# Kernel optimization log

Measured on AMD Instinct MI355X. Metric: run time of the kernel, lower is better.

The kernel has to match this reference:

```python
import jax, jax.numpy as jnp
import numpy as np

N, H, F, E, K = 4096, 512, 2048, 8, 2  # tokens, hidden, ffn(=4H), experts, top_k


def setup_inputs() -> dict:
    key = jax.random.key(0)
    ks = jax.random.split(key, 7)
    def w(k, shape, fan_in):
        return jax.random.normal(k, shape, dtype=jnp.float32) * (fan_in ** -0.5)
    return {
        "x": jax.random.normal(ks[0], (N, H), dtype=jnp.float32),
        "W_in": w(ks[1], (H, H), H),          # input_proj.weight  [out,in]
        "W_router": w(ks[2], (E, H), H),      # router.gate.weight [E,H]
        "W_gate": w(ks[3], (E, F, H), H),     # per-expert gate_proj.weight
        "W_up": w(ks[4], (E, F, H), H),       # per-expert up_proj.weight
        "W_down": w(ks[5], (E, H, F), F),     # per-expert down_proj.weight
        "W_out": w(ks[6], (H, H), H),         # output_proj.weight
    }


def reference(x, W_in, W_router, W_gate, W_up, W_down, W_out):
    h = x @ W_in.T                                  # [N,H] input_proj
    logits = h @ W_router.T                         # [N,E]
    # route_mode='balanced' and world_size==1 -> expert_bias is None
    probs = jax.nn.softmax(logits, axis=-1)
    top_w, top_i = jax.lax.top_k(probs, K)          # [N,K]
    top_w = jax.nn.softmax(top_w, axis=-1)          # renormalize over top-k

    # per-token combine weight for each expert: [N,E]
    onehot = jax.nn.one_hot(top_i, E, dtype=h.dtype)      # [N,K,E]
    combine_w = jnp.einsum('nk,nke->ne', top_w, onehot)

    def expert(wg, wu, wd):
        # SwiGLU FFN: down( silu(gate(h)) * up(h) )
        return (jax.nn.silu(h @ wg.T) * (h @ wu.T)) @ wd.T  # [N,H]

    expert_out = jax.vmap(expert)(W_gate, W_up, W_down)     # [E,N,H]
    combined = jnp.einsum('ne,enh->nh', combine_w, expert_out)
    return combined @ W_out.T                                # output_proj
```

## Files before the change

### kernel.cpp

```cpp
#include <hip/hip_runtime.h>

typedef unsigned short u16;
typedef unsigned int u32;
typedef short bf16x8 __attribute__((ext_vector_type(8)));
typedef float f32x4 __attribute__((ext_vector_type(4)));

#define AS1 __attribute__((address_space(1)))
#define AS3 __attribute__((address_space(3)))

#define NTOK 4096
#define HDIM 512
#define FDIM 2048
#define NEXP 8
#define NASSIGN (NTOK * 2)
#define NPAD2 (NASSIGN + NEXP * 256)
#define RBMAX 128

__device__ __forceinline__ void g2l16(const void* g, void* l) {
  __builtin_amdgcn_global_load_lds((const AS1 u32*)g, (AS3 u32*)l, 16, 0, 0);
}
__device__ __forceinline__ u16 f2bf(float f) {
  u32 u = __float_as_uint(f);
  u = (u + 0x7FFFu + ((u >> 16) & 1u)) >> 16;
  return (u16)u;
}
__device__ __forceinline__ float bf2f(u16 h) { return __uint_as_float(((u32)h) << 16); }

#define WAITV0() asm volatile("s_waitcnt vmcnt(0)" ::: "memory")
#define BAR() __builtin_amdgcn_s_barrier()
#define SCB() __builtin_amdgcn_sched_barrier(0)
#define PRIO1() __builtin_amdgcn_s_setprio(1)
#define PRIO0() __builtin_amdgcn_s_setprio(0)
#define VMBAR() do { WAITV0(); BAR(); } while (0)

__global__ __launch_bounds__(256) void cvtall_kernel(
    const float* __restrict__ x, const float* __restrict__ Wi, const float* __restrict__ Wo,
    const float* __restrict__ Wg, const float* __restrict__ Wu, const float* __restrict__ Wd,
    const float* __restrict__ Wr,
    u16* __restrict__ xb, u16* __restrict__ Wib, u16* __restrict__ Wob,
    u16* __restrict__ Wgb, u16* __restrict__ Wub, u16* __restrict__ Wdb,
    double* __restrict__ wre) {
  const int b = blockIdx.x, tid = threadIdx.x;
  if (b < 6784) {
    const int b4 = b * 1024;
    const float* s; u16* d; int o;
    if (b4 < 524288) { s = x; d = xb; o = b4; }
    else if (b4 < 589824) { s = Wi; d = Wib; o = b4 - 524288; }
    else if (b4 < 655360) { s = Wo; d = Wob; o = b4 - 589824; }
    else if (b4 < 2752512) { s = Wg; d = Wgb; o = b4 - 655360; }
    else if (b4 < 4849664) { s = Wu; d = Wub; o = b4 - 2752512; }
    else { s = Wd; d = Wdb; o = b4 - 4849664; }
    const int oo = o + tid;
    const float4 v0 = ((const float4*)s)[oo];
    const float4 v1 = ((const float4*)s)[oo + 256];
    const float4 v2 = ((const float4*)s)[oo + 512];
    const float4 v3 = ((const float4*)s)[oo + 768];
    ushort4 t0, t1, t2, t3;
    t0.x = f2bf(v0.x); t0.y = f2bf(v0.y); t0.z = f2bf(v0.z); t0.w = f2bf(v0.w);
    t1.x = f2bf(v1.x); t1.y = f2bf(v1.y); t1.z = f2bf(v1.z); t1.w = f2bf(v1.w);
    t2.x = f2bf(v2.x); t2.y = f2bf(v2.y); t2.z = f2bf(v2.z); t2.w = f2bf(v2.w);
    t3.x = f2bf(v3.x); t3.y = f2bf(v3.y); t3.z = f2bf(v3.z); t3.w = f2bf(v3.w);
    ((ushort4*)d)[oo] = t0;
    ((ushort4*)d)[oo + 256] = t1;
    ((ushort4*)d)[oo + 512] = t2;
    ((ushort4*)d)[oo + 768] = t3;
  } else {
    const int t = (b - 6784) * 256 + tid;
    const int e = t >> 9, k = t & 511;
    const float* wr = Wr + e * HDIM;
    double a0 = 0.0, a1 = 0.0, a2 = 0.0, a3 = 0.0;
    for (int j = 0; j < HDIM; j += 4) {
      a0 += (double)wr[j + 0] * (double)Wi[(j + 0) * HDIM + k];
      a1 += (double)wr[j + 1] * (double)Wi[(j + 1) * HDIM + k];
      a2 += (double)wr[j + 2] * (double)Wi[(j + 2) * HDIM + k];
      a3 += (double)wr[j + 3] * (double)Wi[(j + 3) * HDIM + k];
    }
    wre[t] = (a0 + a1) + (a2 + a3);
  }
}

__global__ __launch_bounds__(128) void router_kernel(
    const float* __restrict__ x, const double* __restrict__ wre,
    int* __restrict__ idx, float* __restrict__ wts) {
  __shared__ double lw[NEXP * HDIM];
  for (int i = threadIdx.x; i < NEXP * HDIM; i += 128) lw[i] = wre[i];
  __syncthreads();
  const int n = blockIdx.x * 128 + threadIdx.x;
  const float* xr = x + (size_t)n * HDIM;
  double acc[NEXP] = {};
  for (int k4 = 0; k4 < HDIM / 4; ++k4) {
    const float4 xv = ((const float4*)xr)[k4];
    const float xc[4] = {xv.x, xv.y, xv.z, xv.w};
#pragma unroll
    for (int c = 0; c < 4; ++c) {
      const double xd = (double)xc[c];
#pragma unroll
      for (int e = 0; e < NEXP; ++e) acc[e] += xd * lw[e * HDIM + k4 * 4 + c];
    }
  }
  double mx = acc[0];
#pragma unroll
  for (int e = 1; e < NEXP; ++e) mx = acc[e] > mx ? acc[e] : mx;
  double p[NEXP], se = 0.0;
#pragma unroll
  for (int e = 0; e < NEXP; ++e) { p[e] = exp(acc[e] - mx); se += p[e]; }
  const double inv = 1.0 / se;
#pragma unroll
  for (int e = 0; e < NEXP; ++e) p[e] *= inv;
  int i0 = 0; double b0 = p[0];
#pragma unroll
  for (int e = 1; e < NEXP; ++e) if (p[e] > b0) { b0 = p[e]; i0 = e; }
  int i1 = -1; double b1 = -1.0;
#pragma unroll
  for (int e = 0; e < NEXP; ++e) if (e != i0 && p[e] > b1) { b1 = p[e]; i1 = e; }
  const double e0 = exp(b0), e1 = exp(b1);
  idx[2 * n] = i0; idx[2 * n + 1] = i1;
  wts[2 * n] = (float)(e0 / (e0 + e1));
  wts[2 * n + 1] = (float)(e1 / (e0 + e1));
}

__global__ void assign_kernel(const int* __restrict__ idx, int* __restrict__ tok,
                              int* __restrict__ pos, int* __restrict__ rbe2,
                              int* __restrict__ rbp2, int* __restrict__ rbe1,
                              int* __restrict__ rbp1, int* __restrict__ nrb) {
  __shared__ int cnt[NEXP], cur[NEXP];
  const int tid = threadIdx.x;
  if (tid < NEXP) cnt[tid] = 0;
  __syncthreads();
  for (int a = tid; a < NASSIGN; a += 256) atomicAdd(&cnt[idx[a]], 1);
  __syncthreads();
  if (tid == 0) {
    int o = 0, n2 = 0, n1 = 0;
    for (int e = 0; e < NEXP; ++e) {
      cur[e] = o;
      const int nb2 = (cnt[e] + 255) >> 8;
      const int nb1 = (cnt[e] + 127) >> 7;
      for (int i = 0; i < nb2; ++i) { rbe2[n2] = e; rbp2[n2] = o + i * 256; ++n2; }
      for (int i = 0; i < nb1; ++i) { rbe1[n1] = e; rbp1[n1] = o + i * 128; ++n1; }
      o += nb2 * 256;
    }
    nrb[0] = n2; nrb[1] = n1;
  }
  __syncthreads();
  for (int p = tid; p < NPAD2; p += 256) tok[p] = 0;
  __syncthreads();
  for (int a = tid; a < NASSIGN; a += 256) {
    const int e = idx[a];
    const int q = atomicAdd(&cur[e], 1);
    tok[q] = a >> 1;
    pos[a] = q;
  }
}

template <int SB, int NT>
__device__ __forceinline__ void gemm128_body(
    const u16* __restrict__ A, const u16* __restrict__ B, void* __restrict__ C,
    int m0, int n0, int N, int K, u16* sm, int tid) {
  u16 *lA0 = sm, *lA1 = sm + 8192, *lB0 = sm + 16384, *lB1 = sm + 24576;
  const int w = tid >> 6, l = tid & 63;
  const int wm = (w >> 2) * 64, wn = (w & 3) * 32;
  const int lm = l & 15, lk = (l >> 4) * 8, xr = (l & 7) << 3;
  const int sr = l >> 3, sc = ((l & 7) ^ sr) * 8;
  const u16* As = A + (size_t)(m0 + w * 8 + sr) * K + sc;
  const u16* Bs = B + (size_t)(n0 + w * 8 + sr) * K + sc;
  f32x4 acc[4][2] = {};
  auto STG = [&](u16* dA, u16* dB, int kt) {
    g2l16(As + kt, dA + w * 512);
    g2l16(As + (size_t)64 * K + kt, dA + 4096 + w * 512);
    g2l16(Bs + kt, dB + w * 512);
    g2l16(Bs + (size_t)64 * K + kt, dB + 4096 + w * 512);
  };
  auto CMP = [&](const u16* a_, const u16* b_) {
#pragma unroll
    for (int kk = 0; kk < 2; ++kk) {
      const int ko = (kk * 32 + lk) ^ xr;
      bf16x8 af[4], bf[2];
#pragma unroll
      for (int i = 0; i < 4; ++i) af[i] = *(const bf16x8*)(a_ + (wm + i * 16 + lm) * 64 + ko);
#pragma unroll
      for (int j = 0; j < 2; ++j) bf[j] = *(const bf16x8*)(b_ + (wn + j * 16 + lm) * 64 + ko);
#pragma unroll
      for (int i = 0; i < 4; ++i)
#pragma unroll
        for (int j = 0; j < 2; ++j)
          acc[i][j] = __builtin_amdgcn_mfma_f32_16x16x32_bf16(af[i], bf[j], acc[i][j], 0, 0, 0);
    }
  };
  STG(lA0, lB0, 0);
  VMBAR();
  for (int t = 0; t < NT; t += 2) {
    if (t + 1 < NT) STG(lA1, lB1, (t + 1) * 64);
    CMP(lA0, lB0);
    VMBAR();
    if (t + 2 < NT) STG(lA0, lB0, (t + 2) * 64);
    CMP(lA1, lB1);
    VMBAR();
  }
  const int cr = (l >> 4) * 4, cc = lm;
#pragma unroll
  for (int i = 0; i < 4; ++i)
#pragma unroll
    for (int j = 0; j < 2; ++j)
#pragma unroll
      for (int r = 0; r < 4; ++r) {
        const size_t o = (size_t)(m0 + wm + i * 16 + cr + r) * N + n0 + wn + j * 16 + cc;
        if (SB) ((u16*)C)[o] = f2bf(acc[i][j][r]);
        else ((float*)C)[o] = acc[i][j][r];
      }
}

__global__ __launch_bounds__(512, 2) void ingemm_kernel(
    const u16* __restrict__ xb, const u16* __restrict__ Wib, u16* __restrict__ hb) {
  __shared__ __align__(16) u16 sm[32768];
  gemm128_body<1, 8>(xb, Wib, hb, blockIdx.y * 128, blockIdx.x * 128, HDIM, HDIM, sm, threadIdx.x);
}

__global__ __launch_bounds__(512, 2) void outgemm_kernel(
    const u16* __restrict__ cb, const u16* __restrict__ Wob, float* __restrict__ out) {
  __shared__ __align__(16) u16 sm[32768];
  gemm128_body<0, 8>(cb, Wob, out, blockIdx.y * 128, blockIdx.x * 128, HDIM, HDIM, sm, threadIdx.x);
}

__global__ __launch_bounds__(512, 2) void gateup_kernel(
    const u16* __restrict__ hb, const u16* __restrict__ Wg, const u16* __restrict__ Wu,
    u16* __restrict__ act, const int* __restrict__ tok, const int* __restrict__ rbe2,
    const int* __restrict__ rbp2, const int* __restrict__ nrb) {
  const int rb = blockIdx.y;
  if (rb >= nrb[0]) return;
  __shared__ __align__(16) u16 sm[65536];
  const int e = rbe2[rb], p0 = rbp2[rb], n0 = blockIdx.x * 128;
  const int tid = threadIdx.x, w = tid >> 6, l = tid & 63;
  const int wr = w >> 1, wc = w & 1;
  const int lm = l & 15, lk = (l >> 4) * 8, xr = (l & 7) * 8;
  const int sr = l >> 3, sc = ((l & 7) ^ sr) * 8;
  const int ko0 = lk ^ xr, ko1 = (32 + lk) ^ xr;
  const u16* Asrc[4];
#pragma unroll
  for (int c = 0; c < 4; ++c)
    Asrc[c] = hb + (size_t)tok[p0 + c * 64 + w * 8 + sr] * HDIM + sc;
  const u16 *Gsrc[2], *Usrc[2];
#pragma unroll
  for (int c = 0; c < 2; ++c) {
    Gsrc[c] = Wg + (size_t)e * FDIM * HDIM + (size_t)(n0 + c * 64 + w * 8 + sr) * HDIM + sc;
    Usrc[c] = Wu + (size_t)e * FDIM * HDIM + (size_t)(n0 + c * 64 + w * 8 + sr) * HDIM + sc;
  }
  f32x4 ag[4][4] = {}, au[4][4] = {};
  auto stgA = [&](int b, int kt) {
#pragma unroll
    for (int c = 0; c < 4; ++c) g2l16(Asrc[c] + kt, sm + b * 32768 + c * 4096 + w * 512);
  };
  auto stgGU = [&](int b, int kt) {
#pragma unroll
    for (int c = 0; c < 2; ++c) {
      g2l16(Gsrc[c] + kt, sm + b * 32768 + 16384 + c * 4096 + w * 512);
      g2l16(Usrc[c] + kt, sm + b * 32768 + 24576 + c * 4096 + w * 512);
    }
  };
  stgA(0, 0); stgGU(0, 0);
  WAITV0(); BAR(); SCB();
#pragma unroll 2
  for (int t = 0; t < 8; ++t) {
    const int bu = t & 1, bn = bu ^ 1;
    const u16* A_ = sm + bu * 32768;
    const u16* G_ = A_ + 16384;
    const u16* U_ = A_ + 24576;
    bf16x8 af[4], gf[4], uf[4];
#pragma unroll
    for (int i = 0; i < 4; ++i) af[i] = *(const bf16x8*)(A_ + (wr * 64 + i * 16 + lm) * 64 + ko0);
#pragma unroll
    for (int j = 0; j < 4; ++j) gf[j] = *(const bf16x8*)(G_ + (wc * 64 + j * 16 + lm) * 64 + ko0);
    if (t < 7) stgA(bn, (t + 1) * 64);
    PRIO1();
#pragma unroll
    for (int i = 0; i < 4; ++i)
#pragma unroll
      for (int j = 0; j < 4; ++j)
        ag[i][j] = __builtin_amdgcn_mfma_f32_16x16x32_bf16(af[i], gf[j], ag[i][j], 0, 0, 0);
    PRIO0();
    BAR(); SCB();
#pragma unroll
    for (int j = 0; j < 4; ++j) uf[j] = *(const bf16x8*)(U_ + (wc * 64 + j * 16 + lm) * 64 + ko0);
    if (t < 7) stgGU(bn, (t + 1) * 64);
    PRIO1();
#pragma unroll
    for (int i = 0; i < 4; ++i)
#pragma unroll
      for (int j = 0; j < 4; ++j)
        au[i][j] = __builtin_amdgcn_mfma_f32_16x16x32_bf16(af[i], uf[j], au[i][j], 0, 0, 0);
    PRIO0();
    BAR(); SCB();
#pragma unroll
    for (int i = 0; i < 4; ++i) af[i] = *(const bf16x8*)(A_ + (wr * 64 + i * 16 + lm) * 64 + ko1);
#pragma unroll
    for (int j = 0; j < 4; ++j) gf[j] = *(const bf16x8*)(G_ + (wc * 64 + j * 16 + lm) * 64 + ko1);
    PRIO1();
#pragma unroll
    for (int i = 0; i < 4; ++i)
#pragma unroll
      for (int j = 0; j < 4; ++j)
        ag[i][j] = __builtin_amdgcn_mfma_f32_16x16x32_bf16(af[i], gf[j], ag[i][j], 0, 0, 0);
    PRIO0();
    BAR(); SCB();
#pragma unroll
    for (int j = 0; j < 4; ++j) uf[j] = *(const bf16x8*)(U_ + (wc * 64 + j * 16 + lm) * 64 + ko1);
    PRIO1();
#pragma unroll
    for (int i = 0; i < 4; ++i)
#pragma unroll
      for (int j = 0; j < 4; ++j)
        au[i][j] = __builtin_amdgcn_mfma_f32_16x16x32_bf16(af[i], uf[j], au[i][j], 0, 0, 0);
    PRIO0();
    if (t < 7) WAITV0();
    BAR(); SCB();
  }
  const int cr = (l >> 4) * 4, cc = lm;
#pragma unroll
  for (int i = 0; i < 4; ++i)
#pragma unroll
    for (int j = 0; j < 4; ++j)
#pragma unroll
      for (int r = 0; r < 4; ++r) {
        const float g = ag[i][j][r], u = au[i][j][r];
        const float s = g / (1.0f + __expf(-g));
        act[(size_t)(p0 + wr * 64 + i * 16 + cr + r) * FDIM + n0 + wc * 64 + j * 16 + cc] =
            f2bf(s * u);
      }
}

__global__ __launch_bounds__(256, 2) void down_kernel(
    const u16* __restrict__ act, const u16* __restrict__ Wd, u16* __restrict__ dwn,
    const int* __restrict__ rbe1, const int* __restrict__ rbp1, const int* __restrict__ nrb) {
  const int rb = blockIdx.y;
  if (rb >= nrb[1]) return;
  __shared__ __align__(16) u16 sm[32768];
  const int e = rbe1[rb], p0 = rbp1[rb], n0 = blockIdx.x * 128;
  const int tid = threadIdx.x, w = tid >> 6, l = tid & 63;
  const int wr = w >> 1, wc = w & 1;
  const int lm = l & 15, lk = (l >> 4) * 8, xr = (l & 7) * 8;
  const int sr = l >> 3, sc = ((l & 7) ^ sr) * 8;
  const int ko0 = lk ^ xr, ko1 = (32 + lk) ^ xr;
  const u16 *Asrc[4], *Bsrc[4];
#pragma unroll
  for (int c = 0; c < 4; ++c) {
    Asrc[c] = act + (size_t)(p0 + c * 32 + w * 8 + sr) * FDIM + sc;
    Bsrc[c] = Wd + (size_t)e * HDIM * FDIM + (size_t)(n0 + c * 32 + w * 8 + sr) * FDIM + sc;
  }
  f32x4 acc[4][4] = {};
  auto STG = [&](int b, int kt) {
#pragma unroll
    for (int c = 0; c < 4; ++c) {
      g2l16(Asrc[c] + kt, sm + b * 16384 + c * 2048 + w * 512);
      g2l16(Bsrc[c] + kt, sm + b * 16384 + 8192 + c * 2048 + w * 512);
    }
  };
  STG(0, 0);
  WAITV0(); BAR(); SCB();
#pragma unroll 2
  for (int t = 0; t < 32; ++t) {
    const int bu = t & 1, bn = bu ^ 1;
    const u16* A_ = sm + bu * 16384;
    const u16* B_ = A_ + 8192;
    bf16x8 af[4], bf[4];
#pragma unroll
    for (int i = 0; i < 4; ++i) af[i] = *(const bf16x8*)(A_ + (wr * 64 + i * 16 + lm) * 64 + ko0);
#pragma unroll
    for (int j = 0; j < 4; ++j) bf[j] = *(const bf16x8*)(B_ + (wc * 64 + j * 16 + lm) * 64 + ko0);
    if (t < 31) STG(bn, (t + 1) * 64);
    PRIO1();
#pragma unroll
    for (int i = 0; i < 4; ++i)
#pragma unroll
      for (int j = 0; j < 4; ++j)
        acc[i][j] = __builtin_amdgcn_mfma_f32_16x16x32_bf16(af[i], bf[j], acc[i][j], 0, 0, 0);
    PRIO0();
    BAR(); SCB();
#pragma unroll
    for (int i = 0; i < 4; ++i) af[i] = *(const bf16x8*)(A_ + (wr * 64 + i * 16 + lm) * 64 + ko1);
#pragma unroll
    for (int j = 0; j < 4; ++j) bf[j] = *(const bf16x8*)(B_ + (wc * 64 + j * 16 + lm) * 64 + ko1);
    PRIO1();
#pragma unroll
    for (int i = 0; i < 4; ++i)
#pragma unroll
      for (int j = 0; j < 4; ++j)
        acc[i][j] = __builtin_amdgcn_mfma_f32_16x16x32_bf16(af[i], bf[j], acc[i][j], 0, 0, 0);
    PRIO0();
    if (t < 31) WAITV0();
    BAR(); SCB();
  }
  const int cr = (l >> 4) * 4, cc = lm;
#pragma unroll
  for (int i = 0; i < 4; ++i)
#pragma unroll
    for (int j = 0; j < 4; ++j)
#pragma unroll
      for (int r = 0; r < 4; ++r)
        dwn[(size_t)(p0 + wr * 64 + i * 16 + cr + r) * HDIM + n0 + wc * 64 + j * 16 + cc] =
            f2bf(acc[i][j][r]);
}

__global__ void combine_kernel(const u16* __restrict__ dwn, const int* __restrict__ pos,
                               const float* __restrict__ wts, u16* __restrict__ cb) {
  const int n = blockIdx.x, t = threadIdx.x;
  const int p0 = pos[2 * n], p1 = pos[2 * n + 1];
  const float w0 = wts[2 * n], w1 = wts[2 * n + 1];
  const ushort4 a = ((const ushort4*)(dwn + (size_t)p0 * HDIM))[t];
  const ushort4 b = ((const ushort4*)(dwn + (size_t)p1 * HDIM))[t];
  ushort4 o;
  o.x = f2bf(w0 * bf2f(a.x) + w1 * bf2f(b.x));
  o.y = f2bf(w0 * bf2f(a.y) + w1 * bf2f(b.y));
  o.z = f2bf(w0 * bf2f(a.z) + w1 * bf2f(b.z));
  o.w = f2bf(w0 * bf2f(a.w) + w1 * bf2f(b.w));
  ((ushort4*)(cb + (size_t)n * HDIM))[t] = o;
}

extern "C" void kernel_launch(void* const* d_in, const int* in_sizes, int n_in,
                              void* d_out, int out_size, void* d_ws, size_t ws_size,
                              hipStream_t stream) {
  const float* x  = (const float*)d_in[0];
  const float* Wi = (const float*)d_in[1];
  const float* Wr = (const float*)d_in[2];
  const float* Wg = (const float*)d_in[3];
  const float* Wu = (const float*)d_in[4];
  const float* Wd = (const float*)d_in[5];
  const float* Wo = (const float*)d_in[6];
  float* out = (float*)d_out;

  char* ws = (char*)d_ws;
  size_t off = 0;
  auto alloc = [&](size_t bytes) -> void* {
    off = (off + 255) & ~(size_t)255;
    void* p = ws + off;
    off += bytes;
    return p;
  };
  u16* xb  = (u16*)alloc((size_t)NTOK * HDIM * 2);
  u16* hb  = (u16*)alloc((size_t)NTOK * HDIM * 2);
  u16* cb  = (u16*)alloc((size_t)NTOK * HDIM * 2);
  u16* Wib = (u16*)alloc((size_t)HDIM * HDIM * 2);
  u16* Wob = (u16*)alloc((size_t)HDIM * HDIM * 2);
  u16* Wgb = (u16*)alloc((size_t)NEXP * FDIM * HDIM * 2);
  u16* Wub = (u16*)alloc((size_t)NEXP * FDIM * HDIM * 2);
  u16* Wdb = (u16*)alloc((size_t)NEXP * HDIM * FDIM * 2);
  u16* actb = (u16*)alloc((size_t)NPAD2 * FDIM * 2);
  u16* dwn = (u16*)alloc((size_t)NPAD2 * HDIM * 2);
  double* wre = (double*)alloc((size_t)NEXP * HDIM * 8);
  int* idx = (int*)alloc((size_t)NASSIGN * 4);
  float* wts = (float*)alloc((size_t)NASSIGN * 4);
  int* tok = (int*)alloc((size_t)NPAD2 * 4);
  int* pos = (int*)alloc((size_t)NASSIGN * 4);
  int* rbe2 = (int*)alloc((size_t)RBMAX * 4);
  int* rbp2 = (int*)alloc((size_t)RBMAX * 4);
  int* rbe1 = (int*)alloc((size_t)RBMAX * 4);
  int* rbp1 = (int*)alloc((size_t)RBMAX * 4);
  int* nrb = (int*)alloc(256);

  cvtall_kernel<<<6800, 256, 0, stream>>>(x, Wi, Wo, Wg, Wu, Wd, Wr,
                                          xb, Wib, Wob, Wgb, Wub, Wdb, wre);
  router_kernel<<<32, 128, 0, stream>>>(x, wre, idx, wts);
  assign_kernel<<<1, 256, 0, stream>>>(idx, tok, pos, rbe2, rbp2, rbe1, rbp1, nrb);
  ingemm_kernel<<<dim3(4, 32), 512, 0, stream>>>(xb, Wib, hb);
  gateup_kernel<<<dim3(16, 40), 512, 0, stream>>>(hb, Wgb, Wub, actb, tok, rbe2, rbp2, nrb);
  down_kernel<<<dim3(4, 72), 256, 0, stream>>>(actb, Wdb, dwn, rbe1, rbp1, nrb);
  combine_kernel<<<NTOK, 128, 0, stream>>>(dwn, pos, wts, cb);
  outgemm_kernel<<<dim3(4, 32), 512, 0, stream>>>(cb, Wob, out);
}
```

Before: 224.7 us.

## Fuse fp32-to-bf16 conversion into GEMM operand loads, drop standalone convert pass

Removes the separate pass that converted x and every weight matrix to bf16 in global memory. Each GEMM kernel now loads fp32 operands into registers, packs them to bf16 and writes them to swizzled LDS, while bf16 activations still go through direct global-to-LDS loads. The router-weight precompute moves into its own small kernel. This avoids a full extra read and write of all weights per call, but each GEMM now reads twice the bytes for its weight operand, which adds register pressure and extra wait and sync points in the pipelined loops.

```diff
diff --git a/kernel.cpp b/kernel.cpp
--- a/kernel.cpp
+++ b/kernel.cpp
@@ -1,4 +1,5 @@
 #include <hip/hip_runtime.h>
+#include <hip/hip_bf16.h>
 
 typedef unsigned short u16;
 typedef unsigned int u32;
@@ -25,58 +26,39 @@
   return (u16)u;
 }
 __device__ __forceinline__ float bf2f(u16 h) { return __uint_as_float(((u32)h) << 16); }
-
-#define WAITV0() asm volatile("s_waitcnt vmcnt(0)" ::: "memory")
+__device__ __forceinline__ u32 pkbf(float a, float b) {
+  __hip_bfloat162 h = __float22bfloat162_rn(float2{a, b});
+  u32 r;
+  __builtin_memcpy(&r, &h, 4);
+  return r;
+}
+__device__ __forceinline__ int4 pk8(const float4 a, const float4 b) {
+  int4 r;
+  r.x = (int)pkbf(a.x, a.y); r.y = (int)pkbf(a.z, a.w);
+  r.z = (int)pkbf(b.x, b.y); r.w = (int)pkbf(b.z, b.w);
+  return r;
+}
+
+#define WAITV(N) asm volatile("s_waitcnt vmcnt(" #N ")" ::: "memory")
+#define LGKM0() asm volatile("s_waitcnt lgkmcnt(0)" ::: "memory")
 #define BAR() __builtin_amdgcn_s_barrier()
 #define SCB() __builtin_amdgcn_sched_barrier(0)
 #define PRIO1() __builtin_amdgcn_s_setprio(1)
 #define PRIO0() __builtin_amdgcn_s_setprio(0)
-#define VMBAR() do { WAITV0(); BAR(); } while (0)
-
-__global__ __launch_bounds__(256) void cvtall_kernel(
-    const float* __restrict__ x, const float* __restrict__ Wi, const float* __restrict__ Wo,
-    const float* __restrict__ Wg, const float* __restrict__ Wu, const float* __restrict__ Wd,
-    const float* __restrict__ Wr,
-    u16* __restrict__ xb, u16* __restrict__ Wib, u16* __restrict__ Wob,
-    u16* __restrict__ Wgb, u16* __restrict__ Wub, u16* __restrict__ Wdb,
-    double* __restrict__ wre) {
-  const int b = blockIdx.x, tid = threadIdx.x;
-  if (b < 6784) {
-    const int b4 = b * 1024;
-    const float* s; u16* d; int o;
-    if (b4 < 524288) { s = x; d = xb; o = b4; }
-    else if (b4 < 589824) { s = Wi; d = Wib; o = b4 - 524288; }
-    else if (b4 < 655360) { s = Wo; d = Wob; o = b4 - 589824; }
-    else if (b4 < 2752512) { s = Wg; d = Wgb; o = b4 - 655360; }
-    else if (b4 < 4849664) { s = Wu; d = Wub; o = b4 - 2752512; }
-    else { s = Wd; d = Wdb; o = b4 - 4849664; }
-    const int oo = o + tid;
-    const float4 v0 = ((const float4*)s)[oo];
-    const float4 v1 = ((const float4*)s)[oo + 256];
-    const float4 v2 = ((const float4*)s)[oo + 512];
-    const float4 v3 = ((const float4*)s)[oo + 768];
-    ushort4 t0, t1, t2, t3;
-    t0.x = f2bf(v0.x); t0.y = f2bf(v0.y); t0.z = f2bf(v0.z); t0.w = f2bf(v0.w);
-    t1.x = f2bf(v1.x); t1.y = f2bf(v1.y); t1.z = f2bf(v1.z); t1.w = f2bf(v1.w);
-    t2.x = f2bf(v2.x); t2.y = f2bf(v2.y); t2.z = f2bf(v2.z); t2.w = f2bf(v2.w);
-    t3.x = f2bf(v3.x); t3.y = f2bf(v3.y); t3.z = f2bf(v3.z); t3.w = f2bf(v3.w);
-    ((ushort4*)d)[oo] = t0;
-    ((ushort4*)d)[oo + 256] = t1;
-    ((ushort4*)d)[oo + 512] = t2;
-    ((ushort4*)d)[oo + 768] = t3;
-  } else {
-    const int t = (b - 6784) * 256 + tid;
-    const int e = t >> 9, k = t & 511;
-    const float* wr = Wr + e * HDIM;
-    double a0 = 0.0, a1 = 0.0, a2 = 0.0, a3 = 0.0;
-    for (int j = 0; j < HDIM; j += 4) {
-      a0 += (double)wr[j + 0] * (double)Wi[(j + 0) * HDIM + k];
-      a1 += (double)wr[j + 1] * (double)Wi[(j + 1) * HDIM + k];
-      a2 += (double)wr[j + 2] * (double)Wi[(j + 2) * HDIM + k];
-      a3 += (double)wr[j + 3] * (double)Wi[(j + 3) * HDIM + k];
-    }
-    wre[t] = (a0 + a1) + (a2 + a3);
-  }
+
+__global__ __launch_bounds__(256) void wreff_kernel(
+    const float* __restrict__ Wr, const float* __restrict__ Wi, double* __restrict__ wre) {
+  const int t = blockIdx.x * 256 + threadIdx.x;
+  const int e = t >> 9, k = t & 511;
+  const float* wr = Wr + e * HDIM;
+  double a0 = 0.0, a1 = 0.0, a2 = 0.0, a3 = 0.0;
+  for (int j = 0; j < HDIM; j += 4) {
+    a0 += (double)wr[j + 0] * (double)Wi[(j + 0) * HDIM + k];
+    a1 += (double)wr[j + 1] * (double)Wi[(j + 1) * HDIM + k];
+    a2 += (double)wr[j + 2] * (double)Wi[(j + 2) * HDIM + k];
+    a3 += (double)wr[j + 3] * (double)Wi[(j + 3) * HDIM + k];
+  }
+  wre[t] = (a0 + a1) + (a2 + a3);
 }
 
 __global__ __launch_bounds__(128) void router_kernel(
@@ -152,49 +134,60 @@
   }
 }
 
-template <int SB, int NT>
-__device__ __forceinline__ void gemm128_body(
-    const u16* __restrict__ A, const u16* __restrict__ B, void* __restrict__ C,
-    int m0, int n0, int N, int K, u16* sm, int tid) {
-  u16 *lA0 = sm, *lA1 = sm + 8192, *lB0 = sm + 16384, *lB1 = sm + 24576;
-  const int w = tid >> 6, l = tid & 63;
+__global__ __launch_bounds__(512, 2) void ingemm_kernel(
+    const float* __restrict__ x, const float* __restrict__ Wi, u16* __restrict__ hb) {
+  __shared__ __align__(16) u16 sm[32768];
+  const int m0 = blockIdx.y * 128, n0 = blockIdx.x * 128;
+  const int tid = threadIdx.x, w = tid >> 6, l = tid & 63;
   const int wm = (w >> 2) * 64, wn = (w & 3) * 32;
-  const int lm = l & 15, lk = (l >> 4) * 8, xr = (l & 7) << 3;
-  const int sr = l >> 3, sc = ((l & 7) ^ sr) * 8;
-  const u16* As = A + (size_t)(m0 + w * 8 + sr) * K + sc;
-  const u16* Bs = B + (size_t)(n0 + w * 8 + sr) * K + sc;
+  const int lm = l & 15, lk = (l >> 4) * 8, xr = (l & 7) * 8;
+  const int lr = l >> 3, c8 = l & 7;
+  const int ko0 = lk ^ xr, ko1 = (32 + lk) ^ xr;
+  const int wcol = (c8 ^ lr) * 8;
+  const float* Ap0 = x + (size_t)(m0 + w * 8 + lr) * HDIM + c8 * 8;
+  const float* Ap1 = Ap0 + (size_t)64 * HDIM;
+  const float* Bp0 = Wi + (size_t)(n0 + w * 8 + lr) * HDIM + c8 * 8;
+  const float* Bp1 = Bp0 + (size_t)64 * HDIM;
   f32x4 acc[4][2] = {};
-  auto STG = [&](u16* dA, u16* dB, int kt) {
-    g2l16(As + kt, dA + w * 512);
-    g2l16(As + (size_t)64 * K + kt, dA + 4096 + w * 512);
-    g2l16(Bs + kt, dB + w * 512);
-    g2l16(Bs + (size_t)64 * K + kt, dB + 4096 + w * 512);
-  };
-  auto CMP = [&](const u16* a_, const u16* b_) {
+  float4 v0, v1, v2, v3, v4, v5, v6, v7;
+  auto WLOAD = [&](int kt) {
+    v0 = *(const float4*)(Ap0 + kt); v1 = *(const float4*)(Ap0 + kt + 4);
+    v2 = *(const float4*)(Ap1 + kt); v3 = *(const float4*)(Ap1 + kt + 4);
+    v4 = *(const float4*)(Bp0 + kt); v5 = *(const float4*)(Bp0 + kt + 4);
+    v6 = *(const float4*)(Bp1 + kt); v7 = *(const float4*)(Bp1 + kt + 4);
+  };
+  auto WWRITE = [&](u16* st) {
+    *(int4*)(st + (w * 8 + lr) * 64 + wcol) = pk8(v0, v1);
+    *(int4*)(st + (64 + w * 8 + lr) * 64 + wcol) = pk8(v2, v3);
+    *(int4*)(st + 8192 + (w * 8 + lr) * 64 + wcol) = pk8(v4, v5);
+    *(int4*)(st + 8192 + (64 + w * 8 + lr) * 64 + wcol) = pk8(v6, v7);
+  };
+  WLOAD(0);
+  WAITV(0); WWRITE(sm);
+  LGKM0(); BAR(); SCB();
+  for (int t = 0; t < 8; ++t) {
+    u16* bu = sm + (t & 1) * 16384;
+    u16* bn = sm + ((t + 1) & 1) * 16384;
+    if (t < 7) WLOAD((t + 1) * 64);
+    const u16 *a_ = bu, *b_ = bu + 8192;
 #pragma unroll
     for (int kk = 0; kk < 2; ++kk) {
-      const int ko = (kk * 32 + lk) ^ xr;
+      const int ko = kk ? ko1 : ko0;
       bf16x8 af[4], bf[2];
 #pragma unroll
       for (int i = 0; i < 4; ++i) af[i] = *(const bf16x8*)(a_ + (wm + i * 16 + lm) * 64 + ko);
 #pragma unroll
       for (int j = 0; j < 2; ++j) bf[j] = *(const bf16x8*)(b_ + (wn + j * 16 + lm) * 64 + ko);
+      PRIO1();
 #pragma unroll
       for (int i = 0; i < 4; ++i)
 #pragma unroll
         for (int j = 0; j < 2; ++j)
           acc[i][j] = __builtin_amdgcn_mfma_f32_16x16x32_bf16(af[i], bf[j], acc[i][j], 0, 0, 0);
+      PRIO0();
     }
-  };
-  STG(lA0, lB0, 0);
-  VMBAR();
-  for (int t = 0; t < NT; t += 2) {
-    if (t + 1 < NT) STG(lA1, lB1, (t + 1) * 64);
-    CMP(lA0, lB0);
-    VMBAR();
-    if (t + 2 < NT) STG(lA0, lB0, (t + 2) * 64);
-    CMP(lA1, lB1);
-    VMBAR();
+    if (t < 7) { WAITV(0); WWRITE(bn); }
+    LGKM0(); BAR(); SCB();
   }
   const int cr = (l >> 4) * 4, cc = lm;
 #pragma unroll
@@ -202,27 +195,78 @@
 #pragma unroll
     for (int j = 0; j < 2; ++j)
 #pragma unroll
-      for (int r = 0; r < 4; ++r) {
-        const size_t o = (size_t)(m0 + wm + i * 16 + cr + r) * N + n0 + wn + j * 16 + cc;
-        if (SB) ((u16*)C)[o] = f2bf(acc[i][j][r]);
-        else ((float*)C)[o] = acc[i][j][r];
-      }
-}
-
-__global__ __launch_bounds__(512, 2) void ingemm_kernel(
-    const u16* __restrict__ xb, const u16* __restrict__ Wib, u16* __restrict__ hb) {
+      for (int r = 0; r < 4; ++r)
+        hb[(size_t)(m0 + wm + i * 16 + cr + r) * HDIM + n0 + wn + j * 16 + cc] =
+            f2bf(acc[i][j][r]);
+}
+
+__global__ __launch_bounds__(512, 2) void outgemm_kernel(
+    const u16* __restrict__ cb, const float* __restrict__ Wo, float* __restrict__ out) {
   __shared__ __align__(16) u16 sm[32768];
-  gemm128_body<1, 8>(xb, Wib, hb, blockIdx.y * 128, blockIdx.x * 128, HDIM, HDIM, sm, threadIdx.x);
-}
-
-__global__ __launch_bounds__(512, 2) void outgemm_kernel(
-    const u16* __restrict__ cb, const u16* __restrict__ Wob, float* __restrict__ out) {
-  __shared__ __align__(16) u16 sm[32768];
-  gemm128_body<0, 8>(cb, Wob, out, blockIdx.y * 128, blockIdx.x * 128, HDIM, HDIM, sm, threadIdx.x);
+  const int m0 = blockIdx.y * 128, n0 = blockIdx.x * 128;
+  const int tid = threadIdx.x, w = tid >> 6, l = tid & 63;
+  const int wm = (w >> 2) * 64, wn = (w & 3) * 32;
+  const int lm = l & 15, lk = (l >> 4) * 8, xr = (l & 7) * 8;
+  const int lr = l >> 3, c8 = l & 7;
+  const int ko0 = lk ^ xr, ko1 = (32 + lk) ^ xr;
+  const int wcol = (c8 ^ lr) * 8;
+  const u16* Ap0 = cb + (size_t)(m0 + w * 8 + lr) * HDIM + wcol;
+  const u16* Ap1 = Ap0 + (size_t)64 * HDIM;
+  const float* Bp0 = Wo + (size_t)(n0 + w * 8 + lr) * HDIM + c8 * 8;
+  const float* Bp1 = Bp0 + (size_t)64 * HDIM;
+  f32x4 acc[4][2] = {};
+  float4 v4, v5, v6, v7;
+  auto WLOADB = [&](int kt) {
+    v4 = *(const float4*)(Bp0 + kt); v5 = *(const float4*)(Bp0 + kt + 4);
+    v6 = *(const float4*)(Bp1 + kt); v7 = *(const float4*)(Bp1 + kt + 4);
+  };
+  auto WWRITEB = [&](u16* st) {
+    *(int4*)(st + 8192 + (w * 8 + lr) * 64 + wcol) = pk8(v4, v5);
+    *(int4*)(st + 8192 + (64 + w * 8 + lr) * 64 + wcol) = pk8(v6, v7);
+  };
+  auto STGA = [&](u16* st, int kt) {
+    g2l16(Ap0 + kt, st + w * 512);
+    g2l16(Ap1 + kt, st + 4096 + w * 512);
+  };
+  WLOADB(0); SCB(); STGA(sm, 0);
+  WAITV(2); WWRITEB(sm);
+  WAITV(0); LGKM0(); BAR(); SCB();
+  for (int t = 0; t < 8; ++t) {
+    u16* bu = sm + (t & 1) * 16384;
+    u16* bn = sm + ((t + 1) & 1) * 16384;
+    if (t < 7) { WLOADB((t + 1) * 64); SCB(); STGA(bn, (t + 1) * 64); }
+    const u16 *a_ = bu, *b_ = bu + 8192;
+#pragma unroll
+    for (int kk = 0; kk < 2; ++kk) {
+      const int ko = kk ? ko1 : ko0;
+      bf16x8 af[4], bf[2];
+#pragma unroll
+      for (int i = 0; i < 4; ++i) af[i] = *(const bf16x8*)(a_ + (wm + i * 16 + lm) * 64 + ko);
+#pragma unroll
+      for (int j = 0; j < 2; ++j) bf[j] = *(const bf16x8*)(b_ + (wn + j * 16 + lm) * 64 + ko);
+      PRIO1();
+#pragma unroll
+      for (int i = 0; i < 4; ++i)
+#pragma unroll
+        for (int j = 0; j < 2; ++j)
+          acc[i][j] = __builtin_amdgcn_mfma_f32_16x16x32_bf16(af[i], bf[j], acc[i][j], 0, 0, 0);
+      PRIO0();
+    }
+    if (t < 7) { WAITV(2); WWRITEB(bn); WAITV(0); }
+    LGKM0(); BAR(); SCB();
+  }
+  const int cr = (l >> 4) * 4, cc = lm;
+#pragma unroll
+  for (int i = 0; i < 4; ++i)
+#pragma unroll
+    for (int j = 0; j < 2; ++j)
+#pragma unroll
+      for (int r = 0; r < 4; ++r)
+        out[(size_t)(m0 + wm + i * 16 + cr + r) * HDIM + n0 + wn + j * 16 + cc] = acc[i][j][r];
 }
 
 __global__ __launch_bounds__(512, 2) void gateup_kernel(
-    const u16* __restrict__ hb, const u16* __restrict__ Wg, const u16* __restrict__ Wu,
+    const u16* __restrict__ hb, const float* __restrict__ Wg, const float* __restrict__ Wu,
     u16* __restrict__ act, const int* __restrict__ tok, const int* __restrict__ rbe2,
     const int* __restrict__ rbp2, const int* __restrict__ nrb) {
   const int rb = blockIdx.y;
@@ -232,44 +276,51 @@
   const int tid = threadIdx.x, w = tid >> 6, l = tid & 63;
   const int wr = w >> 1, wc = w & 1;
   const int lm = l & 15, lk = (l >> 4) * 8, xr = (l & 7) * 8;
-  const int sr = l >> 3, sc = ((l & 7) ^ sr) * 8;
+  const int lr = l >> 3, c8 = l & 7;
   const int ko0 = lk ^ xr, ko1 = (32 + lk) ^ xr;
+  const int wcol = (c8 ^ lr) * 8;
   const u16* Asrc[4];
 #pragma unroll
   for (int c = 0; c < 4; ++c)
-    Asrc[c] = hb + (size_t)tok[p0 + c * 64 + w * 8 + sr] * HDIM + sc;
-  const u16 *Gsrc[2], *Usrc[2];
-#pragma unroll
-  for (int c = 0; c < 2; ++c) {
-    Gsrc[c] = Wg + (size_t)e * FDIM * HDIM + (size_t)(n0 + c * 64 + w * 8 + sr) * HDIM + sc;
-    Usrc[c] = Wu + (size_t)e * FDIM * HDIM + (size_t)(n0 + c * 64 + w * 8 + sr) * HDIM + sc;
-  }
+    Asrc[c] = hb + (size_t)tok[p0 + c * 64 + w * 8 + lr] * HDIM + wcol;
+  const float* Gp0 = Wg + (size_t)e * FDIM * HDIM + (size_t)(n0 + w * 8 + lr) * HDIM + c8 * 8;
+  const float* Gp1 = Gp0 + (size_t)64 * HDIM;
+  const float* Up0 = Wu + (size_t)e * FDIM * HDIM + (size_t)(n0 + w * 8 + lr) * HDIM + c8 * 8;
+  const float* Up1 = Up0 + (size_t)64 * HDIM;
   f32x4 ag[4][4] = {}, au[4][4] = {};
-  auto stgA = [&](int b, int kt) {
-#pragma unroll
-    for (int c = 0; c < 4; ++c) g2l16(Asrc[c] + kt, sm + b * 32768 + c * 4096 + w * 512);
-  };
-  auto stgGU = [&](int b, int kt) {
-#pragma unroll
-    for (int c = 0; c < 2; ++c) {
-      g2l16(Gsrc[c] + kt, sm + b * 32768 + 16384 + c * 4096 + w * 512);
-      g2l16(Usrc[c] + kt, sm + b * 32768 + 24576 + c * 4096 + w * 512);
-    }
-  };
-  stgA(0, 0); stgGU(0, 0);
-  WAITV0(); BAR(); SCB();
+  float4 g0, g1, g2, g3, u0, u1, u2, u3;
+  auto WLOAD = [&](int kt) {
+    g0 = *(const float4*)(Gp0 + kt); g1 = *(const float4*)(Gp0 + kt + 4);
+    g2 = *(const float4*)(Gp1 + kt); g3 = *(const float4*)(Gp1 + kt + 4);
+    u0 = *(const float4*)(Up0 + kt); u1 = *(const float4*)(Up0 + kt + 4);
+    u2 = *(const float4*)(Up1 + kt); u3 = *(const float4*)(Up1 + kt + 4);
+  };
+  auto WWRITE = [&](u16* st) {
+    u16* dG = st + 16384;
+    u16* dU = st + 24576;
+    *(int4*)(dG + (w * 8 + lr) * 64 + wcol) = pk8(g0, g1);
+    *(int4*)(dG + (64 + w * 8 + lr) * 64 + wcol) = pk8(g2, g3);
+    *(int4*)(dU + (w * 8 + lr) * 64 + wcol) = pk8(u0, u1);
+    *(int4*)(dU + (64 + w * 8 + lr) * 64 + wcol) = pk8(u2, u3);
+  };
+  auto STGA = [&](u16* st, int kt) {
+#pragma unroll
+    for (int c = 0; c < 4; ++c) g2l16(Asrc[c] + kt, st + c * 4096 + w * 512);
+  };
+  WLOAD(0); SCB(); STGA(sm, 0);
+  WAITV(4); WWRITE(sm);
+  WAITV(0); LGKM0(); BAR(); SCB();
 #pragma unroll 2
   for (int t = 0; t < 8; ++t) {
-    const int bu = t & 1, bn = bu ^ 1;
-    const u16* A_ = sm + bu * 32768;
-    const u16* G_ = A_ + 16384;
-    const u16* U_ = A_ + 24576;
+    u16* bu = sm + (t & 1) * 32768;
+    u16* bn = sm + ((t + 1) & 1) * 32768;
+    const u16 *A_ = bu, *G_ = bu + 16384, *U_ = bu + 24576;
     bf16x8 af[4], gf[4], uf[4];
 #pragma unroll
     for (int i = 0; i < 4; ++i) af[i] = *(const bf16x8*)(A_ + (wr * 64 + i * 16 + lm) * 64 + ko0);
 #pragma unroll
     for (int j = 0; j < 4; ++j) gf[j] = *(const bf16x8*)(G_ + (wc * 64 + j * 16 + lm) * 64 + ko0);
-    if (t < 7) stgA(bn, (t + 1) * 64);
+    if (t < 7) WLOAD((t + 1) * 64);
     PRIO1();
 #pragma unroll
     for (int i = 0; i < 4; ++i)
@@ -280,7 +331,7 @@
     BAR(); SCB();
 #pragma unroll
     for (int j = 0; j < 4; ++j) uf[j] = *(const bf16x8*)(U_ + (wc * 64 + j * 16 + lm) * 64 + ko0);
-    if (t < 7) stgGU(bn, (t + 1) * 64);
+    if (t < 7) STGA(bn, (t + 1) * 64);
     PRIO1();
 #pragma unroll
     for (int i = 0; i < 4; ++i)
@@ -293,6 +344,7 @@
     for (int i = 0; i < 4; ++i) af[i] = *(const bf16x8*)(A_ + (wr * 64 + i * 16 + lm) * 64 + ko1);
 #pragma unroll
     for (int j = 0; j < 4; ++j) gf[j] = *(const bf16x8*)(G_ + (wc * 64 + j * 16 + lm) * 64 + ko1);
+    if (t < 7) { WAITV(4); WWRITE(bn); }
     PRIO1();
 #pragma unroll
     for (int i = 0; i < 4; ++i)
@@ -310,8 +362,8 @@
       for (int j = 0; j < 4; ++j)
         au[i][j] = __builtin_amdgcn_mfma_f32_16x16x32_bf16(af[i], uf[j], au[i][j], 0, 0, 0);
     PRIO0();
-    if (t < 7) WAITV0();
-    BAR(); SCB();
+    if (t < 7) WAITV(0);
+    LGKM0(); BAR(); SCB();
   }
   const int cr = (l >> 4) * 4, cc = lm;
 #pragma unroll
@@ -328,7 +380,7 @@
 }
 
 __global__ __launch_bounds__(256, 2) void down_kernel(
-    const u16* __restrict__ act, const u16* __restrict__ Wd, u16* __restrict__ dwn,
+    const u16* __restrict__ act, const float* __restrict__ Wd, u16* __restrict__ dwn,
     const int* __restrict__ rbe1, const int* __restrict__ rbp1, const int* __restrict__ nrb) {
   const int rb = blockIdx.y;
   if (rb >= nrb[1]) return;
@@ -337,35 +389,50 @@
   const int tid = threadIdx.x, w = tid >> 6, l = tid & 63;
   const int wr = w >> 1, wc = w & 1;
   const int lm = l & 15, lk = (l >> 4) * 8, xr = (l & 7) * 8;
-  const int sr = l >> 3, sc = ((l & 7) ^ sr) * 8;
+  const int lr = l >> 3, c8 = l & 7;
   const int ko0 = lk ^ xr, ko1 = (32 + lk) ^ xr;
-  const u16 *Asrc[4], *Bsrc[4];
-#pragma unroll
-  for (int c = 0; c < 4; ++c) {
-    Asrc[c] = act + (size_t)(p0 + c * 32 + w * 8 + sr) * FDIM + sc;
-    Bsrc[c] = Wd + (size_t)e * HDIM * FDIM + (size_t)(n0 + c * 32 + w * 8 + sr) * FDIM + sc;
-  }
+  const int wcol = (c8 ^ lr) * 8;
+  const u16* Asrc[4];
+#pragma unroll
+  for (int c = 0; c < 4; ++c)
+    Asrc[c] = act + (size_t)(p0 + c * 32 + w * 8 + lr) * FDIM + wcol;
+  const float* Bp[4];
+#pragma unroll
+  for (int c = 0; c < 4; ++c)
+    Bp[c] = Wd + (size_t)e * HDIM * FDIM + (size_t)(n0 + c * 32 + w * 8 + lr) * FDIM + c8 * 8;
   f32x4 acc[4][4] = {};
-  auto STG = [&](int b, int kt) {
-#pragma unroll
-    for (int c = 0; c < 4; ++c) {
-      g2l16(Asrc[c] + kt, sm + b * 16384 + c * 2048 + w * 512);
-      g2l16(Bsrc[c] + kt, sm + b * 16384 + 8192 + c * 2048 + w * 512);
-    }
-  };
-  STG(0, 0);
-  WAITV0(); BAR(); SCB();
+  float4 b0, b1, b2, b3, b4, b5, b6, b7;
+  auto WLOAD = [&](int kt) {
+    b0 = *(const float4*)(Bp[0] + kt); b1 = *(const float4*)(Bp[0] + kt + 4);
+    b2 = *(const float4*)(Bp[1] + kt); b3 = *(const float4*)(Bp[1] + kt + 4);
+    b4 = *(const float4*)(Bp[2] + kt); b5 = *(const float4*)(Bp[2] + kt + 4);
+    b6 = *(const float4*)(Bp[3] + kt); b7 = *(const float4*)(Bp[3] + kt + 4);
+  };
+  auto WWRITE = [&](u16* st) {
+    u16* dB = st + 8192;
+    *(int4*)(dB + (w * 8 + lr) * 64 + wcol) = pk8(b0, b1);
+    *(int4*)(dB + (32 + w * 8 + lr) * 64 + wcol) = pk8(b2, b3);
+    *(int4*)(dB + (64 + w * 8 + lr) * 64 + wcol) = pk8(b4, b5);
+    *(int4*)(dB + (96 + w * 8 + lr) * 64 + wcol) = pk8(b6, b7);
+  };
+  auto STGA = [&](u16* st, int kt) {
+#pragma unroll
+    for (int c = 0; c < 4; ++c) g2l16(Asrc[c] + kt, st + c * 2048 + w * 512);
+  };
+  WLOAD(0); SCB(); STGA(sm, 0);
+  WAITV(4); WWRITE(sm);
+  WAITV(0); LGKM0(); BAR(); SCB();
 #pragma unroll 2
   for (int t = 0; t < 32; ++t) {
-    const int bu = t & 1, bn = bu ^ 1;
-    const u16* A_ = sm + bu * 16384;
-    const u16* B_ = A_ + 8192;
+    u16* bu = sm + (t & 1) * 16384;
+    u16* bn = sm + ((t + 1) & 1) * 16384;
+    const u16 *A_ = bu, *B_ = bu + 8192;
     bf16x8 af[4], bf[4];
 #pragma unroll
     for (int i = 0; i < 4; ++i) af[i] = *(const bf16x8*)(A_ + (wr * 64 + i * 16 + lm) * 64 + ko0);
 #pragma unroll
     for (int j = 0; j < 4; ++j) bf[j] = *(const bf16x8*)(B_ + (wc * 64 + j * 16 + lm) * 64 + ko0);
-    if (t < 31) STG(bn, (t + 1) * 64);
+    if (t < 31) { WLOAD((t + 1) * 64); SCB(); STGA(bn, (t + 1) * 64); }
     PRIO1();
 #pragma unroll
     for (int i = 0; i < 4; ++i)
@@ -378,6 +445,7 @@
     for (int i = 0; i < 4; ++i) af[i] = *(const bf16x8*)(A_ + (wr * 64 + i * 16 + lm) * 64 + ko1);
 #pragma unroll
     for (int j = 0; j < 4; ++j) bf[j] = *(const bf16x8*)(B_ + (wc * 64 + j * 16 + lm) * 64 + ko1);
+    if (t < 31) { WAITV(4); WWRITE(bn); }
     PRIO1();
 #pragma unroll
     for (int i = 0; i < 4; ++i)
@@ -385,8 +453,8 @@
       for (int j = 0; j < 4; ++j)
         acc[i][j] = __builtin_amdgcn_mfma_f32_16x16x32_bf16(af[i], bf[j], acc[i][j], 0, 0, 0);
     PRIO0();
-    if (t < 31) WAITV0();
-    BAR(); SCB();
+    if (t < 31) WAITV(0);
+    LGKM0(); BAR(); SCB();
   }
   const int cr = (l >> 4) * 4, cc = lm;
 #pragma unroll
@@ -434,16 +502,10 @@
     off += bytes;
     return p;
   };
-  u16* xb  = (u16*)alloc((size_t)NTOK * HDIM * 2);
-  u16* hb  = (u16*)alloc((size_t)NTOK * HDIM * 2);
-  u16* cb  = (u16*)alloc((size_t)NTOK * HDIM * 2);
-  u16* Wib = (u16*)alloc((size_t)HDIM * HDIM * 2);
-  u16* Wob = (u16*)alloc((size_t)HDIM * HDIM * 2);
-  u16* Wgb = (u16*)alloc((size_t)NEXP * FDIM * HDIM * 2);
-  u16* Wub = (u16*)alloc((size_t)NEXP * FDIM * HDIM * 2);
-  u16* Wdb = (u16*)alloc((size_t)NEXP * HDIM * FDIM * 2);
+  u16* hb   = (u16*)alloc((size_t)NTOK * HDIM * 2);
+  u16* cb   = (u16*)alloc((size_t)NTOK * HDIM * 2);
   u16* actb = (u16*)alloc((size_t)NPAD2 * FDIM * 2);
-  u16* dwn = (u16*)alloc((size_t)NPAD2 * HDIM * 2);
+  u16* dwn  = (u16*)alloc((size_t)NPAD2 * HDIM * 2);
   double* wre = (double*)alloc((size_t)NEXP * HDIM * 8);
   int* idx = (int*)alloc((size_t)NASSIGN * 4);
   float* wts = (float*)alloc((size_t)NASSIGN * 4);
@@ -455,13 +517,12 @@
   int* rbp1 = (int*)alloc((size_t)RBMAX * 4);
   int* nrb = (int*)alloc(256);
 
-  cvtall_kernel<<<6800, 256, 0, stream>>>(x, Wi, Wo, Wg, Wu, Wd, Wr,
-                                          xb, Wib, Wob, Wgb, Wub, Wdb, wre);
+  wreff_kernel<<<16, 256, 0, stream>>>(Wr, Wi, wre);
   router_kernel<<<32, 128, 0, stream>>>(x, wre, idx, wts);
   assign_kernel<<<1, 256, 0, stream>>>(idx, tok, pos, rbe2, rbp2, rbe1, rbp1, nrb);
-  ingemm_kernel<<<dim3(4, 32), 512, 0, stream>>>(xb, Wib, hb);
-  gateup_kernel<<<dim3(16, 40), 512, 0, stream>>>(hb, Wgb, Wub, actb, tok, rbe2, rbp2, nrb);
-  down_kernel<<<dim3(4, 72), 256, 0, stream>>>(actb, Wdb, dwn, rbe1, rbp1, nrb);
+  ingemm_kernel<<<dim3(4, 32), 512, 0, stream>>>(x, Wi, hb);
+  gateup_kernel<<<dim3(16, 40), 512, 0, stream>>>(hb, Wg, Wu, actb, tok, rbe2, rbp2, nrb);
+  down_kernel<<<dim3(4, 72), 256, 0, stream>>>(actb, Wd, dwn, rbe1, rbp1, nrb);
   combine_kernel<<<NTOK, 128, 0, stream>>>(dwn, pos, wts, cb);
-  outgemm_kernel<<<dim3(4, 32), 512, 0, stream>>>(cb, Wob, out);
-}
+  outgemm_kernel<<<dim3(4, 32), 512, 0, stream>>>(cb, Wo, out);
+}
```

After: 269.3 us. 1.2x slower.
